# Kernel optimization log

Hardware: AMD Instinct MI355X
Metric: run time of the kernel (lower is better)

Reference implementation:

```python
import jax, jax.numpy as jnp
import numpy as np

B, V, F_IN, F_HID = 1000000, 9, 5, 3


def setup_inputs() -> dict:
    key = jax.random.key(0)
    k1, k2, k3, k4, k5 = jax.random.split(key, 5)
    A = jax.random.uniform(k1, (B, V, V), dtype=jnp.float32)
    h0 = jax.random.uniform(k2, (B, V, F_IN), dtype=jnp.float32)
    # learned params (match torch init scales loosely)
    W = jax.random.uniform(k3, (F_IN, F_HID), dtype=jnp.float32) * 0.01
    fc_w = jax.random.normal(k4, (F_HID, 1), dtype=jnp.float32) * 0.1
    fc_b = jnp.zeros((1,), dtype=jnp.float32)
    return {"A": A, "h0": h0, "W": W, "fc_w": fc_w, "fc_b": fc_b}


def reference(A, h0, W, fc_w, fc_b):
    # GCN layer, batched (replaces per-sample Python loop)
    V_ = A.shape[-1]
    AI = A + jnp.eye(V_, dtype=A.dtype)                 # A + I, [B,V,V]
    deg = jnp.sum(AI, axis=-2)                          # torch.sum(AI, 0): column sums, [B,V]
    dinv = 1.0 / jnp.sqrt(deg)                          # diag of D^{-1/2}
    DAD = dinv[..., :, None] * AI * dinv[..., None, :]  # D^-1/2 (A+I) D^-1/2
    HW = jnp.einsum('bvf,fh->bvh', h0, W)               # H W
    h1 = jax.nn.relu(jnp.einsum('bvu,buh->bvh', DAD, HW))
    # graph pooling: sum over nodes
    h2 = jnp.sum(h1, axis=1)                            # [B, F_HID]
    return h2 @ fc_w + fc_b                             # [B, 1]
```

## Files before the change

kernel.cpp:

```cpp
#include <hip/hip_runtime.h>

#define NV 9
#define FIN 5
#define FHID 3
#define SPB 64
#define A_ELEMS (NV*NV)
#define H_ELEMS (NV*FIN)
#define A_CHUNK (SPB*A_ELEMS)
#define H_CHUNK (SPB*H_ELEMS)
#define PERSIST_BLOCKS 512

__device__ __forceinline__ void load_lds16(const float* g, float* l) {
    __builtin_amdgcn_global_load_lds(
        (const __attribute__((address_space(1))) unsigned int*)g,
        (__attribute__((address_space(3))) unsigned int*)l, 16, 0, 0);
}

__device__ __forceinline__ void stage_chunk(const float* __restrict__ gA,
                                            const float* __restrict__ gH,
                                            float* bA, float* bH,
                                            int tid, int cnt)
{
    if (cnt == SPB) {
#pragma unroll
        for (int j = 0; j < 20; j++)
            load_lds16(gA + j * 256 + tid * 4, bA + j * 256 + tid * 4);
        if (tid < 16)
            load_lds16(gA + 20 * 256 + tid * 4, bA + 20 * 256 + tid * 4);
#pragma unroll
        for (int j = 0; j < 11; j++)
            load_lds16(gH + j * 256 + tid * 4, bH + j * 256 + tid * 4);
        if (tid < 16)
            load_lds16(gH + 11 * 256 + tid * 4, bH + 11 * 256 + tid * 4);
    } else {
        const int nA = cnt * A_ELEMS;
        for (int i = tid; i < nA; i += SPB) bA[i] = gA[i];
        const int nH = cnt * H_ELEMS;
        for (int i = tid; i < nH; i += SPB) bH[i] = gH[i];
    }
}

__global__ __launch_bounds__(64) void gcn_fused_kernel(
    const float* __restrict__ A, const float* __restrict__ h0,
    const float* __restrict__ W, const float* __restrict__ fc_w,
    const float* __restrict__ fc_b, float* __restrict__ out, int Btot)
{
    __shared__ float sA[2][A_CHUNK];
    __shared__ float sH[2][H_CHUNK];

    const int tid = threadIdx.x;
    const int nChunks = (Btot + SPB - 1) / SPB;
    int c = blockIdx.x;
    if (c >= nChunks) return;
    const int stride = gridDim.x;

    float Wr[FIN * FHID];
#pragma unroll
    for (int i = 0; i < FIN * FHID; i++) Wr[i] = W[i];
    const float fw0 = fc_w[0], fw1 = fc_w[1], fw2 = fc_w[2];
    const float fb = fc_b[0];

    {
        const long long base = (long long)c * SPB;
        const int cnt = (Btot - (int)base < SPB) ? (Btot - (int)base) : SPB;
        stage_chunk(A + base * A_ELEMS, h0 + base * H_ELEMS, sA[0], sH[0], tid, cnt);
    }
    int cur = 0;

    for (; c < nChunks; c += stride) {
        asm volatile("s_waitcnt vmcnt(0)" ::: "memory");
        __syncthreads();

        const int cn = c + stride;
        if (cn < nChunks) {
            const long long nb = (long long)cn * SPB;
            const int ncnt = (Btot - (int)nb < SPB) ? (Btot - (int)nb) : SPB;
            stage_chunk(A + nb * A_ELEMS, h0 + nb * H_ELEMS,
                        sA[cur ^ 1], sH[cur ^ 1], tid, ncnt);
        }

        const long long base = (long long)c * SPB;
        const int cnt = (Btot - (int)base < SPB) ? (Btot - (int)base) : SPB;

        if (tid < cnt) {
            const float* Ai = sA[cur] + tid * A_ELEMS;
            const float* Hi = sH[cur] + tid * H_ELEMS;

            float a[A_ELEMS];
#pragma unroll
            for (int i = 0; i < A_ELEMS; i++) a[i] = Ai[i];

            float deg[NV];
#pragma unroll
            for (int j = 0; j < NV; j++) deg[j] = 1.0f;
#pragma unroll
            for (int i = 0; i < NV; i++) {
#pragma unroll
                for (int j = 0; j < NV; j++) deg[j] += a[i * NV + j];
            }
            float dinv[NV];
#pragma unroll
            for (int j = 0; j < NV; j++) dinv[j] = 1.0f / sqrtf(deg[j]);

            float G[NV * FHID];
#pragma unroll
            for (int u = 0; u < NV; u++) {
                float hr[FIN];
#pragma unroll
                for (int f = 0; f < FIN; f++) hr[f] = Hi[u * FIN + f];
#pragma unroll
                for (int h = 0; h < FHID; h++) {
                    float acc = 0.0f;
#pragma unroll
                    for (int f = 0; f < FIN; f++) acc += hr[f] * Wr[f * FHID + h];
                    G[u * FHID + h] = dinv[u] * acc;
                }
            }

            float h2_0 = 0.0f, h2_1 = 0.0f, h2_2 = 0.0f;
#pragma unroll
            for (int v = 0; v < NV; v++) {
                float a0 = 0.0f, a1 = 0.0f, a2 = 0.0f;
#pragma unroll
                for (int u = 0; u < NV; u++) {
                    float aiv = a[v * NV + u] + ((u == v) ? 1.0f : 0.0f);
                    a0 += aiv * G[u * FHID + 0];
                    a1 += aiv * G[u * FHID + 1];
                    a2 += aiv * G[u * FHID + 2];
                }
                const float dv = dinv[v];
                a0 *= dv; a1 *= dv; a2 *= dv;
                h2_0 += fmaxf(a0, 0.0f);
                h2_1 += fmaxf(a1, 0.0f);
                h2_2 += fmaxf(a2, 0.0f);
            }

            out[base + tid] = h2_0 * fw0 + h2_1 * fw1 + h2_2 * fw2 + fb;
        }
        cur ^= 1;
    }
}

extern "C" void kernel_launch(void* const* d_in, const int* in_sizes, int n_in,
                              void* d_out, int out_size, void* d_ws, size_t ws_size,
                              hipStream_t stream) {
    const float* A    = (const float*)d_in[0];
    const float* h0   = (const float*)d_in[1];
    const float* W    = (const float*)d_in[2];
    const float* fc_w = (const float*)d_in[3];
    const float* fc_b = (const float*)d_in[4];
    float* out = (float*)d_out;

    const int Btot = in_sizes[0] / A_ELEMS;
    const int nChunks = (Btot + SPB - 1) / SPB;
    const int grid = nChunks < PERSIST_BLOCKS ? nChunks : PERSIST_BLOCKS;

    gcn_fused_kernel<<<grid, SPB, 0, stream>>>(A, h0, W, fc_w, fc_b, out, Btot);
}
```

Measured before the change: 550.1 us.

## Single-buffer LDS with register-staged prefetch and more persistent blocks per CU

Replaces the double-buffered LDS staging with a single buffer. Each wave copies its A and H data (and HW) from LDS into registers, waits for those LDS reads, then issues the async global-to-LDS prefetch of the next chunk into the same buffer while it computes degrees and aggregation from registers. Halving LDS per block allows more resident blocks, and the persistent grid grows from 512 to 256*5 blocks to raise memory-level parallelism for this bandwidth-bound kernel. The cost is higher register pressure from keeping the A tile and G live across the prefetch issue.

```diff
diff --git a/kernel.cpp b/kernel.cpp
--- a/kernel.cpp
+++ b/kernel.cpp
@@ -8,7 +8,8 @@
 #define H_ELEMS (NV*FIN)
 #define A_CHUNK (SPB*A_ELEMS)
 #define H_CHUNK (SPB*H_ELEMS)
-#define PERSIST_BLOCKS 512
+#define SLOTS_PER_CU 5
+#define PERSIST_BLOCKS (256*SLOTS_PER_CU)
 
 __device__ __forceinline__ void load_lds16(const float* g, float* l) {
     __builtin_amdgcn_global_load_lds(
@@ -40,13 +41,13 @@
     }
 }
 
-__global__ __launch_bounds__(64) void gcn_fused_kernel(
+__global__ __launch_bounds__(64) void gcn_persist_kernel(
     const float* __restrict__ A, const float* __restrict__ h0,
     const float* __restrict__ W, const float* __restrict__ fc_w,
     const float* __restrict__ fc_b, float* __restrict__ out, int Btot)
 {
-    __shared__ float sA[2][A_CHUNK];
-    __shared__ float sH[2][H_CHUNK];
+    __shared__ float sA[A_CHUNK];
+    __shared__ float sH[H_CHUNK];
 
     const int tid = threadIdx.x;
     const int nChunks = (Btot + SPB - 1) / SPB;
@@ -56,53 +57,30 @@
 
     float Wr[FIN * FHID];
 #pragma unroll
-    for (int i = 0; i < FIN * FHID; i++) Wr[i] = W[i];
+    for (int k = 0; k < FIN * FHID; k++) Wr[k] = W[k];
     const float fw0 = fc_w[0], fw1 = fc_w[1], fw2 = fc_w[2];
     const float fb = fc_b[0];
 
     {
         const long long base = (long long)c * SPB;
         const int cnt = (Btot - (int)base < SPB) ? (Btot - (int)base) : SPB;
-        stage_chunk(A + base * A_ELEMS, h0 + base * H_ELEMS, sA[0], sH[0], tid, cnt);
+        stage_chunk(A + base * A_ELEMS, h0 + base * H_ELEMS, sA, sH, tid, cnt);
     }
-    int cur = 0;
 
     for (; c < nChunks; c += stride) {
-        asm volatile("s_waitcnt vmcnt(0)" ::: "memory");
-        __syncthreads();
-
-        const int cn = c + stride;
-        if (cn < nChunks) {
-            const long long nb = (long long)cn * SPB;
-            const int ncnt = (Btot - (int)nb < SPB) ? (Btot - (int)nb) : SPB;
-            stage_chunk(A + nb * A_ELEMS, h0 + nb * H_ELEMS,
-                        sA[cur ^ 1], sH[cur ^ 1], tid, ncnt);
-        }
+        asm volatile("s_waitcnt vmcnt(0) lgkmcnt(0)" ::: "memory");
 
         const long long base = (long long)c * SPB;
         const int cnt = (Btot - (int)base < SPB) ? (Btot - (int)base) : SPB;
+        const bool active = tid < cnt;
 
-        if (tid < cnt) {
-            const float* Ai = sA[cur] + tid * A_ELEMS;
-            const float* Hi = sH[cur] + tid * H_ELEMS;
-
-            float a[A_ELEMS];
+        float a[A_ELEMS];
+        float G[NV * FHID];
+        if (active) {
+            const float* Ai = sA + tid * A_ELEMS;
+            const float* Hi = sH + tid * H_ELEMS;
 #pragma unroll
             for (int i = 0; i < A_ELEMS; i++) a[i] = Ai[i];
-
-            float deg[NV];
-#pragma unroll
-            for (int j = 0; j < NV; j++) deg[j] = 1.0f;
-#pragma unroll
-            for (int i = 0; i < NV; i++) {
-#pragma unroll
-                for (int j = 0; j < NV; j++) deg[j] += a[i * NV + j];
-            }
-            float dinv[NV];
-#pragma unroll
-            for (int j = 0; j < NV; j++) dinv[j] = 1.0f / sqrtf(deg[j]);
-
-            float G[NV * FHID];
 #pragma unroll
             for (int u = 0; u < NV; u++) {
                 float hr[FIN];
@@ -113,8 +91,37 @@
                     float acc = 0.0f;
 #pragma unroll
                     for (int f = 0; f < FIN; f++) acc += hr[f] * Wr[f * FHID + h];
-                    G[u * FHID + h] = dinv[u] * acc;
+                    G[u * FHID + h] = acc;
                 }
+            }
+        }
+
+        asm volatile("s_waitcnt lgkmcnt(0)" ::: "memory");
+
+        const int cn = c + stride;
+        if (cn < nChunks) {
+            const long long nb = (long long)cn * SPB;
+            const int ncnt = (Btot - (int)nb < SPB) ? (Btot - (int)nb) : SPB;
+            stage_chunk(A + nb * A_ELEMS, h0 + nb * H_ELEMS, sA, sH, tid, ncnt);
+        }
+
+        if (active) {
+            float deg[NV];
+#pragma unroll
+            for (int j = 0; j < NV; j++) deg[j] = 1.0f;
+#pragma unroll
+            for (int r = 0; r < NV; r++) {
+#pragma unroll
+                for (int j = 0; j < NV; j++) deg[j] += a[r * NV + j];
+            }
+            float dinv[NV];
+#pragma unroll
+            for (int j = 0; j < NV; j++) dinv[j] = 1.0f / sqrtf(deg[j]);
+
+#pragma unroll
+            for (int u = 0; u < NV; u++) {
+#pragma unroll
+                for (int h = 0; h < FHID; h++) G[u * FHID + h] *= dinv[u];
             }
 
             float h2_0 = 0.0f, h2_1 = 0.0f, h2_2 = 0.0f;
@@ -123,21 +130,19 @@
                 float a0 = 0.0f, a1 = 0.0f, a2 = 0.0f;
 #pragma unroll
                 for (int u = 0; u < NV; u++) {
-                    float aiv = a[v * NV + u] + ((u == v) ? 1.0f : 0.0f);
+                    const float aiv = a[v * NV + u] + ((u == v) ? 1.0f : 0.0f);
                     a0 += aiv * G[u * FHID + 0];
                     a1 += aiv * G[u * FHID + 1];
                     a2 += aiv * G[u * FHID + 2];
                 }
                 const float dv = dinv[v];
-                a0 *= dv; a1 *= dv; a2 *= dv;
-                h2_0 += fmaxf(a0, 0.0f);
-                h2_1 += fmaxf(a1, 0.0f);
-                h2_2 += fmaxf(a2, 0.0f);
+                h2_0 += fmaxf(a0 * dv, 0.0f);
+                h2_1 += fmaxf(a1 * dv, 0.0f);
+                h2_2 += fmaxf(a2 * dv, 0.0f);
             }
 
             out[base + tid] = h2_0 * fw0 + h2_1 * fw1 + h2_2 * fw2 + fb;
         }
-        cur ^= 1;
     }
 }
 
@@ -155,5 +160,5 @@
     const int nChunks = (Btot + SPB - 1) / SPB;
     const int grid = nChunks < PERSIST_BLOCKS ? nChunks : PERSIST_BLOCKS;
 
-    gcn_fused_kernel<<<grid, SPB, 0, stream>>>(A, h0, W, fc_w, fc_b, out, Btot);
+    gcn_persist_kernel<<<grid, SPB, 0, stream>>>(A, h0, W, fc_w, fc_b, out, Btot);
 }
```

Result: slower. 563.3 us (+2.4%).
